# Kernel tuning notes

Measured on AMD Instinct MI355X. Metric: run time of the kernel, lower is better.

Reference implementation:

```python
import jax, jax.numpy as jnp
import numpy as np

D_IN = 1024
D_OUT = 1024
NUM_HEADS = 16
HEAD_DIM = D_OUT // NUM_HEADS


def setup_inputs() -> dict:
    key = jax.random.key(0)
    ks = jax.random.split(key, 6)
    scale = 1.0 / np.sqrt(D_IN)
    x = jax.random.normal(ks[0], (4, 2048, D_IN), dtype=jnp.float32)
    # nn.Linear stores weight as [out, in]; we keep [in, out] for x @ W
    W_query = jax.random.uniform(ks[1], (D_IN, D_OUT), jnp.float32, -scale, scale)
    W_key = jax.random.uniform(ks[2], (D_IN, D_OUT), jnp.float32, -scale, scale)
    W_value = jax.random.uniform(ks[3], (D_IN, D_OUT), jnp.float32, -scale, scale)
    W_out = jax.random.uniform(ks[4], (D_OUT, D_OUT), jnp.float32, -scale, scale)
    b_out = jax.random.uniform(ks[5], (D_OUT,), jnp.float32, -scale, scale)
    return {"x": x, "W_query": W_query, "W_key": W_key, "W_value": W_value,
            "W_out": W_out, "b_out": b_out}


def reference(x, W_query, W_key, W_value, W_out, b_out):
    b, n, _ = x.shape
    # QKV projections -> [b, h, n, d]
    def proj(W):
        return (x @ W).reshape(b, n, NUM_HEADS, HEAD_DIM).transpose(0, 2, 1, 3)
    q = proj(W_query)
    k = proj(W_key)
    v = proj(W_value)
    # scaled scores [b, h, n, n] with causal mask
    scores = jnp.einsum('bhqd,bhkd->bhqk', q, k) / jnp.sqrt(jnp.float32(HEAD_DIM))
    causal = jnp.tril(jnp.ones((n, n), dtype=bool))
    scores = jnp.where(causal, scores, -jnp.inf)
    weights = jax.nn.softmax(scores, axis=-1)  # dropout p=0.0 -> identity
    ctx = jnp.einsum('bhqk,bhkd->bhqd', weights, v)
    ctx = ctx.transpose(0, 2, 1, 3).reshape(b, n, D_OUT)
    return ctx @ W_out + b_out
```

## Files before the change

### kernel.cpp

```cpp
#include <hip/hip_runtime.h>
#include <hip/hip_bf16.h>
#include <math.h>


typedef __bf16  bf16x8  __attribute__((ext_vector_type(8)));
typedef __bf16  bf16x2  __attribute__((ext_vector_type(2)));
typedef float   floatx4 __attribute__((ext_vector_type(4)));
typedef short   shortx4 __attribute__((ext_vector_type(4)));

#if __has_builtin(__builtin_amdgcn_mfma_f32_16x16x16bf16_1k)
#define HAVE_MFMA16 1
#endif

__device__ __forceinline__ unsigned short f2bf(float f) {
    __hip_bfloat16 h = __float2bfloat16(f);
    return *reinterpret_cast<unsigned short*>(&h);
}

__device__ __forceinline__ unsigned int pkbf(float a, float b) {
#if __has_builtin(__builtin_amdgcn_cvt_pk_bf16_f32)
    bf16x2 t = __builtin_amdgcn_cvt_pk_bf16_f32(a, b);
    return __builtin_bit_cast(unsigned int, t);
#else
    return (unsigned int)f2bf(a) | ((unsigned int)f2bf(b) << 16);
#endif
}
__device__ __forceinline__ ushort4 pk4(float a, float b, float c, float d) {
    union { ushort4 u; unsigned int w[2]; } u;
    u.w[0] = pkbf(a, b);
    u.w[1] = pkbf(c, d);
    return u.u;
}

__device__ __forceinline__ void gll16(const unsigned short* g, unsigned short* l) {
    __builtin_amdgcn_global_load_lds(
        (const __attribute__((address_space(1))) unsigned int*)g,
        (__attribute__((address_space(3))) unsigned int*)l, 16, 0, 0);
}

__global__ void prep(const float* __restrict__ x, unsigned short* __restrict__ xb,
                     const float* __restrict__ Wq, const float* __restrict__ Wk,
                     const float* __restrict__ Wv, const float* __restrict__ Wo,
                     unsigned short* __restrict__ WT, unsigned short* __restrict__ WoT) {
    __shared__ float tile[32][33];
    int bid = blockIdx.x, tid = threadIdx.x;
    if (bid < 8192) {
        int i = (bid * 256 + tid) * 4;
        float4 v = *(const float4*)(x + i);
        *(ushort4*)(xb + i) = pk4(v.x, v.y, v.z, v.w);
        return;
    }
    int id = bid - 8192;
    int mat = id >> 10, rem = id & 1023;
    const float* src = (mat == 0) ? Wq : (mat == 1) ? Wk : (mat == 2) ? Wv : Wo;
    unsigned short* dst = (mat < 3) ? WT : WoT;
    int nbase = (mat < 3) ? mat * 1024 : 0;
    int kt = (rem & 31) * 32, nt = (rem >> 5) * 32;
    int tx = tid & 31, ty = tid >> 5;
    for (int j = 0; j < 32; j += 8)
        tile[ty + j][tx] = src[(kt + ty + j) * 1024 + nt + tx];
    __syncthreads();
    for (int j = 0; j < 32; j += 8) {
        int n = nt + ty + j;
        dst[(nbase + n) * 1024 + kt + tx] = f2bf(tile[tx][ty + j]);
    }
}

template <int EPI>
__global__ __launch_bounds__(256) void gemm_bt(const unsigned short* __restrict__ A,
                                               const unsigned short* __restrict__ B,
                                               unsigned short* __restrict__ Qo,
                                               unsigned short* __restrict__ Ko,
                                               unsigned short* __restrict__ Vo,
                                               const float* __restrict__ bias,
                                               float* __restrict__ Out) {
    __shared__ __align__(16) unsigned short As[128 * 64];
    __shared__ __align__(16) unsigned short Bs[128 * 64];

    int tid = threadIdx.x;
    int lane = tid & 63, w = tid >> 6;
    int wm = w >> 1, wn = w & 1;
    int lm = lane & 15, quad = lane >> 4;
    int m0 = blockIdx.x * 128, n0 = blockIdx.y * 128;
    bool sw = (EPI == 1) || (n0 < 2048);

    floatx4 acc[4][4] = {};

    for (int kb = 0; kb < 1024; kb += 64) {
        __syncthreads();
        for (int p = 0; p < 4; ++p) {
            int id = p * 256 + tid;
            int row = id >> 3;
            int cbs = ((id & 7) ^ (row & 7)) * 8;
            int lbase = (p * 256 + w * 64) * 8;
            gll16(&A[(m0 + row) * 1024 + kb + cbs], &As[lbase]);
            gll16(&B[(n0 + row) * 1024 + kb + cbs], &Bs[lbase]);
        }
        __syncthreads();
        bf16x8 af[2][4], bf[2][4];
        for (int ks = 0; ks < 2; ++ks)
            for (int i = 0; i < 4; ++i) {
                int pu = (((ks * 4 + quad) ^ (lm & 7))) * 8;
                af[ks][i] = *(const bf16x8*)&As[(wm * 64 + i * 16 + lm) * 64 + pu];
                bf[ks][i] = *(const bf16x8*)&Bs[(wn * 64 + i * 16 + lm) * 64 + pu];
            }
        if (sw) {
            for (int mi = 0; mi < 4; ++mi)
                for (int ni = 0; ni < 4; ++ni) {
                    acc[mi][ni] = __builtin_amdgcn_mfma_f32_16x16x32_bf16(bf[0][ni], af[0][mi], acc[mi][ni], 0, 0, 0);
                    acc[mi][ni] = __builtin_amdgcn_mfma_f32_16x16x32_bf16(bf[1][ni], af[1][mi], acc[mi][ni], 0, 0, 0);
                }
        } else {
            for (int mi = 0; mi < 4; ++mi)
                for (int ni = 0; ni < 4; ++ni) {
                    acc[mi][ni] = __builtin_amdgcn_mfma_f32_16x16x32_bf16(af[0][mi], bf[0][ni], acc[mi][ni], 0, 0, 0);
                    acc[mi][ni] = __builtin_amdgcn_mfma_f32_16x16x32_bf16(af[1][mi], bf[1][ni], acc[mi][ni], 0, 0, 0);
                }
        }
    }

    if constexpr (EPI == 0) {
        if (sw) {
            bool isQ = (n0 < 1024);
            unsigned short* dst = isQ ? Qo : Ko;
            float qs = isQ ? 0.1803368801f : 1.0f;
            for (int mi = 0; mi < 4; ++mi) {
                int s = m0 + wm * 64 + mi * 16 + lm;
                int bb = s >> 11, sl = s & 2047;
                for (int ni = 0; ni < 4; ++ni) {
                    int gcol0 = n0 + wn * 64 + ni * 16 + quad * 4;
                    int h = (gcol0 & 1023) >> 6, d0 = gcol0 & 63;
                    *(ushort4*)&dst[(((size_t)(bb * 16 + h) * 2048) + sl) * 64 + d0] =
                        pk4(acc[mi][ni][0] * qs, acc[mi][ni][1] * qs,
                            acc[mi][ni][2] * qs, acc[mi][ni][3] * qs);
                }
            }
        } else {
            for (int mi = 0; mi < 4; ++mi) {
                int grow0 = m0 + wm * 64 + mi * 16 + quad * 4;
                int bb = grow0 >> 11, sl = grow0 & 2047;
                for (int ni = 0; ni < 4; ++ni) {
                    int gcol = n0 + wn * 64 + ni * 16 + lm;
                    int hn = gcol & 1023;
                    int h = hn >> 6, d = hn & 63;
                    *(ushort4*)&Vo[((size_t)(bb * 16 + h) * 64 + d) * 2048 + sl] =
                        pk4(acc[mi][ni][0], acc[mi][ni][1], acc[mi][ni][2], acc[mi][ni][3]);
                }
            }
        }
    } else {
        for (int mi = 0; mi < 4; ++mi) {
            int s = m0 + wm * 64 + mi * 16 + lm;
            for (int ni = 0; ni < 4; ++ni) {
                int gcol0 = n0 + wn * 64 + ni * 16 + quad * 4;
                float4 bv = *(const float4*)&bias[gcol0];
                float4 o;
                o.x = acc[mi][ni][0] + bv.x; o.y = acc[mi][ni][1] + bv.y;
                o.z = acc[mi][ni][2] + bv.z; o.w = acc[mi][ni][3] + bv.w;
                *(float4*)&Out[(size_t)s * 1024 + gcol0] = o;
            }
        }
    }
}

__global__ __launch_bounds__(512) void attn(const unsigned short* __restrict__ Q,
                                            const unsigned short* __restrict__ K,
                                            const unsigned short* __restrict__ Vt,
                                            unsigned short* __restrict__ ctx) {
    constexpr int LKS = 72;
    __shared__ __align__(16) unsigned short Ks[2][64 * LKS];
    __shared__ __align__(16) unsigned short Vts[2][64 * LKS];

    int tid = threadIdx.x, lane = tid & 63, w = tid >> 6;
    int lm = lane & 15, quad = lane >> 4;
    int blk = blockIdx.x;
    int bh = blk & 63;
    int qt = 15 - (blk >> 6);
    int trips = 2 * qt + 2;
    int tmax = 2 * qt + (w >> 2);
    const unsigned short* Qg  = Q  + (size_t)bh * 2048 * 64;
    const unsigned short* Kg  = K  + (size_t)bh * 2048 * 64;
    const unsigned short* Vtg = Vt + (size_t)bh * 64 * 2048;

    int qrow = qt * 128 + w * 16 + lm;
    bf16x8 aq0 = *(const bf16x8*)&Qg[qrow * 64 + quad * 8];
    bf16x8 aq1 = *(const bf16x8*)&Qg[qrow * 64 + 32 + quad * 8];

    floatx4 O[4] = {};
    float lrow = 0.f;

    int r0 = tid >> 3, c0 = (tid & 7) * 8;

    {
        uint4 k0 = *(const uint4*)&Kg[r0 * 64 + c0];
        uint4 v0 = *(const uint4*)&Vtg[r0 * 2048 + c0];
        *(uint4*)&Ks[0][r0 * LKS + c0]  = k0;
        *(uint4*)&Vts[0][r0 * LKS + c0] = v0;
    }
    __syncthreads();

    for (int t = 0; t < trips; ++t) {
        int cur = t & 1, nxt = cur ^ 1;
        bool pre = (t + 1 < trips);
        uint4 pk, pv;
        if (pre) {
            int kb2 = (t + 1) * 64;
            pk = *(const uint4*)&Kg[(kb2 + r0) * 64 + c0];
            pv = *(const uint4*)&Vtg[r0 * 2048 + kb2 + c0];
        }

        if (t <= tmax) {
            const unsigned short* Kc = Ks[cur];
            const unsigned short* Vc = Vts[cur];

            floatx4 s[4];
            for (int n = 0; n < 4; ++n) {
                bf16x8 a0 = *(const bf16x8*)&Kc[(n * 16 + lm) * LKS + quad * 8];
                bf16x8 a1 = *(const bf16x8*)&Kc[(n * 16 + lm) * LKS + 32 + quad * 8];
                floatx4 z = {};
                z = __builtin_amdgcn_mfma_f32_16x16x32_bf16(a0, aq0, z, 0, 0, 0);
                z = __builtin_amdgcn_mfma_f32_16x16x32_bf16(a1, aq1, z, 0, 0, 0);
                s[n] = z;
            }

            bool diag = (t == tmax);
            if (diag) {
                int qr = (w & 3) * 16 + lm;
                for (int n = 0; n < 4; ++n)
                    for (int r = 0; r < 4; ++r)
                        if (n * 16 + quad * 4 + r > qr) s[n][r] = -INFINITY;
            }
            float p[4][4], rs = 0.f;
            for (int n = 0; n < 4; ++n)
                for (int r = 0; r < 4; ++r) {
                    p[n][r] = __builtin_amdgcn_exp2f(s[n][r]);
                    rs += p[n][r];
                }
            lrow += rs;

#ifdef HAVE_MFMA16
            shortx4 pb[4];
            for (int n = 0; n < 4; ++n) {
                union { shortx4 s4; unsigned int w2[2]; } u;
                u.w2[0] = pkbf(p[n][0], p[n][1]);
                u.w2[1] = pkbf(p[n][2], p[n][3]);
                pb[n] = u.s4;
            }
            for (int dblk = 0; dblk < 4; ++dblk)
                for (int n = 0; n < 4; ++n) {
                    shortx4 va = *(const shortx4*)&Vc[(dblk * 16 + lm) * LKS + n * 16 + quad * 4];
                    O[dblk] = __builtin_amdgcn_mfma_f32_16x16x16bf16_1k(va, pb[n], O[dblk], 0, 0, 0);
                }
#else
            unsigned int dw[4][2];
            for (int n = 0; n < 4; ++n) {
                dw[n][0] = pkbf(p[n][0], p[n][1]);
                dw[n][1] = pkbf(p[n][2], p[n][3]);
            }
            bool hiTile = (quad >> 1);
            for (int hh = 0; hh < 2; ++hh) {
                unsigned int bp[4];
                for (int j = 0; j < 4; ++j) {
                    int srcLane = lm + (((quad & 1) * 2 + (j >> 1)) << 4);
                    unsigned int lo = __shfl((int)dw[2 * hh][j & 1], srcLane);
                    unsigned int hi = __shfl((int)dw[2 * hh + 1][j & 1], srcLane);
                    bp[j] = hiTile ? hi : lo;
                }
                bf16x8 bfrag = *(bf16x8*)bp;
                for (int dblk = 0; dblk < 4; ++dblk) {
                    bf16x8 av = *(const bf16x8*)&Vc[(dblk * 16 + lm) * LKS + hh * 32 + quad * 8];
                    O[dblk] = __builtin_amdgcn_mfma_f32_16x16x32_bf16(av, bfrag, O[dblk], 0, 0, 0);
                }
            }
#endif
        }

        if (pre) {
            *(uint4*)&Ks[nxt][r0 * LKS + c0]  = pk;
            *(uint4*)&Vts[nxt][r0 * LKS + c0] = pv;
        }
        __syncthreads();
    }

    lrow += __shfl_xor(lrow, 16);
    lrow += __shfl_xor(lrow, 32);

    int b = bh >> 4, h = bh & 15;
    int q = qt * 128 + w * 16 + lm;
    float inv = 1.0f / lrow;
    for (int dblk = 0; dblk < 4; ++dblk) {
        *(ushort4*)&ctx[((size_t)(b * 2048 + q)) * 1024 + h * 64 + dblk * 16 + quad * 4] =
            pk4(O[dblk][0] * inv, O[dblk][1] * inv, O[dblk][2] * inv, O[dblk][3] * inv);
    }
}

extern "C" void kernel_launch(void* const* d_in, const int* in_sizes, int n_in,
                              void* d_out, int out_size, void* d_ws, size_t ws_size,
                              hipStream_t stream) {
    const float* x   = (const float*)d_in[0];
    const float* Wq  = (const float*)d_in[1];
    const float* Wk  = (const float*)d_in[2];
    const float* Wv  = (const float*)d_in[3];
    const float* Wo  = (const float*)d_in[4];
    const float* bo  = (const float*)d_in[5];
    float* out = (float*)d_out;

    char* ws = (char*)d_ws;
    unsigned short* xb  = (unsigned short*)(ws);
    unsigned short* WT  = (unsigned short*)(ws + 16777216);
    unsigned short* WoT = (unsigned short*)(ws + 23068672);
    unsigned short* Qb  = (unsigned short*)(ws + 25165824);
    unsigned short* Kb  = (unsigned short*)(ws + 41943040);
    unsigned short* Vtb = (unsigned short*)(ws + 58720256);
    unsigned short* ctx = xb;

    prep<<<12288, 256, 0, stream>>>(x, xb, Wq, Wk, Wv, Wo, WT, WoT);
    gemm_bt<0><<<dim3(64, 24), 256, 0, stream>>>(xb, WT, Qb, Kb, Vtb, nullptr, nullptr);
    attn<<<1024, 512, 0, stream>>>(Qb, Kb, Vtb, ctx);
    gemm_bt<1><<<dim3(64, 8), 256, 0, stream>>>(ctx, WoT, nullptr, nullptr, nullptr, bo, out);
}
```

Measured before the change: 254.7 us.

## Replace QKV projection GEMM with 256x256-tile double-buffered 8-wave kernel

Adds a dedicated QKV projection kernel that uses 256x256 output tiles with 8 waves, double-buffered LDS staging through direct global-to-LDS loads, XOR-swizzled shared layout, and 16x16x32 bf16 MFMA with priority hints. It also remaps block IDs for L2 locality and swaps MFMA operand order for the Q/K output so stores are row-contiguous. The goal is to raise arithmetic intensity and overlap loads with compute compared with the 128x128 single-buffered GEMM. In exchange it uses 128KB of LDS per block with heavy register pressure, which limits occupancy.

```diff
diff --git a/kernel.cpp b/kernel.cpp
--- a/kernel.cpp
+++ b/kernel.cpp
@@ -63,6 +63,145 @@
     for (int j = 0; j < 32; j += 8) {
         int n = nt + ty + j;
         dst[(nbase + n) * 1024 + kt + tx] = f2bf(tile[tx][ty + j]);
+    }
+}
+
+#define FENCE asm volatile("" ::: "memory")
+
+#define LDA_FRAG(dst, MQ)                                              \
+    _Pragma("unroll") for (int ks_ = 0; ks_ < 2; ++ks_)                \
+    _Pragma("unroll") for (int i_ = 0; i_ < 4; ++i_) {                 \
+        int row_ = wm * 128 + (MQ) * 64 + i_ * 16 + lm;                \
+        int pu_ = ((ks_ * 4 + quad) ^ (lm & 7)) * 8;                   \
+        dst[ks_][i_] = *(const bf16x8*)&Ac[row_ * 64 + pu_];           \
+    }
+
+#define LDB_FRAG(dst, NQ)                                              \
+    _Pragma("unroll") for (int ks_ = 0; ks_ < 2; ++ks_)                \
+    _Pragma("unroll") for (int j_ = 0; j_ < 2; ++j_) {                 \
+        int row_ = wn * 64 + (NQ) * 32 + j_ * 16 + lm;                 \
+        int pu_ = ((ks_ * 4 + quad) ^ (lm & 7)) * 8;                   \
+        dst[ks_][j_] = *(const bf16x8*)&Bc[row_ * 64 + pu_];           \
+    }
+
+#define MMA_Q(afr, bfr, MQ, NQ)                                                            \
+    __builtin_amdgcn_s_setprio(1);                                                         \
+    if (sw) {                                                                              \
+        _Pragma("unroll") for (int i_ = 0; i_ < 4; ++i_)                                   \
+        _Pragma("unroll") for (int j_ = 0; j_ < 2; ++j_) {                                 \
+            floatx4& c_ = acc[(MQ) * 4 + i_][(NQ) * 2 + j_];                               \
+            c_ = __builtin_amdgcn_mfma_f32_16x16x32_bf16(bfr[0][j_], afr[0][i_], c_, 0, 0, 0); \
+            c_ = __builtin_amdgcn_mfma_f32_16x16x32_bf16(bfr[1][j_], afr[1][i_], c_, 0, 0, 0); \
+        }                                                                                  \
+    } else {                                                                               \
+        _Pragma("unroll") for (int i_ = 0; i_ < 4; ++i_)                                   \
+        _Pragma("unroll") for (int j_ = 0; j_ < 2; ++j_) {                                 \
+            floatx4& c_ = acc[(MQ) * 4 + i_][(NQ) * 2 + j_];                               \
+            c_ = __builtin_amdgcn_mfma_f32_16x16x32_bf16(afr[0][i_], bfr[0][j_], c_, 0, 0, 0); \
+            c_ = __builtin_amdgcn_mfma_f32_16x16x32_bf16(afr[1][i_], bfr[1][j_], c_, 0, 0, 0); \
+        }                                                                                  \
+    }                                                                                      \
+    __builtin_amdgcn_s_setprio(0);
+
+__global__ __launch_bounds__(512, 2) void gemm_qkv(const unsigned short* __restrict__ A,
+                                                   const unsigned short* __restrict__ B,
+                                                   unsigned short* __restrict__ Qo,
+                                                   unsigned short* __restrict__ Ko,
+                                                   unsigned short* __restrict__ Vo) {
+    __shared__ __align__(16) unsigned short As[2][256 * 64];
+    __shared__ __align__(16) unsigned short Bs[2][256 * 64];
+
+    int tid = threadIdx.x;
+    int lane = tid & 63, w = tid >> 6;
+    int wm = w >> 2, wn = w & 3;
+    int lm = lane & 15, quad = lane >> 4;
+
+    int bid = blockIdx.x;
+    int swz = (bid & 7) * 48 + (bid >> 3);
+    int bm = swz / 12, bn = swz % 12;
+    int m0 = bm * 256, n0 = bn * 256;
+    bool sw = (n0 < 2048);
+
+    const unsigned short* Ag = A + (size_t)m0 * 1024;
+    const unsigned short* Bg = B + (size_t)n0 * 1024;
+
+    auto STAGE = [&](int bufi, int kb) {
+#pragma unroll
+        for (int p = 0; p < 4; ++p) {
+            int id = p * 512 + tid;
+            int row = id >> 3;
+            int cbs = ((id & 7) ^ (row & 7)) * 8;
+            int lofs = (p * 512 + w * 64) * 8;
+            gll16(&Ag[row * 1024 + kb + cbs], &As[bufi][lofs]);
+            gll16(&Bg[row * 1024 + kb + cbs], &Bs[bufi][lofs]);
+        }
+    };
+
+    floatx4 acc[8][4] = {};
+
+    STAGE(0, 0);
+    STAGE(1, 64);
+    asm volatile("s_waitcnt vmcnt(8)" ::: "memory");
+    FENCE; __builtin_amdgcn_s_barrier(); FENCE;
+
+#pragma unroll 1
+    for (int t = 0; t < 16; ++t) {
+        const unsigned short* Ac = As[t & 1];
+        const unsigned short* Bc = Bs[t & 1];
+        bf16x8 a0[2][4], a1[2][4], b0[2][2], b1[2][2];
+
+        LDA_FRAG(a0, 0);
+        LDB_FRAG(b0, 0);
+        MMA_Q(a0, b0, 0, 0);
+        __builtin_amdgcn_s_barrier();
+        LDB_FRAG(b1, 1);
+        MMA_Q(a0, b1, 0, 1);
+        __builtin_amdgcn_s_barrier();
+        LDA_FRAG(a1, 1);
+        MMA_Q(a1, b1, 1, 1);
+        __builtin_amdgcn_s_barrier();
+        MMA_Q(a1, b0, 1, 0);
+
+        FENCE; __builtin_amdgcn_s_barrier(); FENCE;
+        if (t + 2 < 16) STAGE(t & 1, (t + 2) * 64);
+        if (t + 1 < 16) {
+            if (t + 2 < 16) { asm volatile("s_waitcnt vmcnt(8)" ::: "memory"); }
+            else            { asm volatile("s_waitcnt vmcnt(0)" ::: "memory"); }
+            FENCE; __builtin_amdgcn_s_barrier(); FENCE;
+        }
+    }
+
+    if (sw) {
+        bool isQ = (n0 < 1024);
+        unsigned short* dst = isQ ? Qo : Ko;
+        float qs = isQ ? 0.1803368801f : 1.0f;
+#pragma unroll
+        for (int mi = 0; mi < 8; ++mi) {
+            int s = m0 + wm * 128 + mi * 16 + lm;
+            int bb = s >> 11, sl = s & 2047;
+#pragma unroll
+            for (int ni = 0; ni < 4; ++ni) {
+                int gcol0 = n0 + wn * 64 + ni * 16 + quad * 4;
+                int h = (gcol0 & 1023) >> 6, d0 = gcol0 & 63;
+                *(ushort4*)&dst[(((size_t)(bb * 16 + h) * 2048) + sl) * 64 + d0] =
+                    pk4(acc[mi][ni][0] * qs, acc[mi][ni][1] * qs,
+                        acc[mi][ni][2] * qs, acc[mi][ni][3] * qs);
+            }
+        }
+    } else {
+#pragma unroll
+        for (int mi = 0; mi < 8; ++mi) {
+            int grow0 = m0 + wm * 128 + mi * 16 + quad * 4;
+            int bb = grow0 >> 11, sl = grow0 & 2047;
+#pragma unroll
+            for (int ni = 0; ni < 4; ++ni) {
+                int gcol = n0 + wn * 64 + ni * 16 + lm;
+                int hn = gcol & 1023;
+                int h = hn >> 6, d = hn & 63;
+                *(ushort4*)&Vo[((size_t)(bb * 16 + h) * 64 + d) * 2048 + sl] =
+                    pk4(acc[mi][ni][0], acc[mi][ni][1], acc[mi][ni][2], acc[mi][ni][3]);
+            }
+        }
     }
 }
 
@@ -315,7 +454,7 @@
     unsigned short* ctx = xb;
 
     prep<<<12288, 256, 0, stream>>>(x, xb, Wq, Wk, Wv, Wo, WT, WoT);
-    gemm_bt<0><<<dim3(64, 24), 256, 0, stream>>>(xb, WT, Qb, Kb, Vtb, nullptr, nullptr);
+    gemm_qkv<<<384, 512, 0, stream>>>(xb, WT, Qb, Kb, Vtb);
     attn<<<1024, 512, 0, stream>>>(Qb, Kb, Vtb, ctx);
     gemm_bt<1><<<dim3(64, 8), 256, 0, stream>>>(ctx, WoT, nullptr, nullptr, nullptr, bo, out);
 }
```

After: 265.9 us. 1.04x slower.
